# Optimization experiments

Measured on AMD Instinct MI355X. Metric: run time of the kernel, lower is better.

The kernel has to match this reference:

```python
import jax, jax.numpy as jnp
import numpy as np

N = 100000        # nodes
E = 1600000       # edges
DIM = 64
HEADS = 8
HEAD_DIM = DIM // HEADS
HIDDEN = 4 * DIM  # hidden_dim_multiplier = 4


def setup_inputs() -> dict:
    key = jax.random.key(0)
    ks = jax.random.split(key, 20)
    s = 0.05
    return {
        "x": jax.random.normal(ks[0], (N, DIM), jnp.float32),
        "edge_feat": jax.random.normal(ks[1], (E, 2), jnp.float32),
        "w_in": jax.random.normal(ks[2], (DIM, DIM), jnp.float32) * s,
        "b_in": jnp.zeros((DIM,), jnp.float32),
        "w_edge": jax.random.normal(ks[3], (2, DIM), jnp.float32) * s,
        "b_edge": jnp.zeros((DIM,), jnp.float32),
        "w_att_u": jax.random.normal(ks[4], (DIM, HEADS), jnp.float32) * s,
        "b_att_u": jnp.zeros((HEADS,), jnp.float32),
        "w_att_v": jax.random.normal(ks[5], (DIM, HEADS), jnp.float32) * s,  # no bias
        "w_att_e": jax.random.normal(ks[6], (DIM, HEADS), jnp.float32) * s,
        "b_att_e": jnp.zeros((HEADS,), jnp.float32),
        "w_ff1": jax.random.normal(ks[7], (DIM, HIDDEN), jnp.float32) * s,
        "b_ff1": jnp.zeros((HIDDEN,), jnp.float32),
        "w_ff2": jax.random.normal(ks[8], (HIDDEN, DIM), jnp.float32) * s,
        "b_ff2": jnp.zeros((DIM,), jnp.float32),
        "src": jax.random.randint(ks[9], (E,), 0, N, jnp.int32),
        "dst": jax.random.randint(ks[10], (E,), 0, N, jnp.int32),
    }


def reference(x, edge_feat, w_in, b_in, w_edge, b_edge, w_att_u, b_att_u,
              w_att_v, w_att_e, b_att_e, w_ff1, b_ff1, w_ff2, b_ff2, src, dst):
    n = x.shape[0]
    h = x @ w_in + b_in                                  # [N, dim]
    ea = edge_feat @ w_edge + b_edge                     # [E, dim]
    su = h @ w_att_u + b_att_u                           # [N, H]
    sv = h @ w_att_v                                     # [N, H] (no bias)
    se = ea @ w_att_e + b_att_e                          # [E, H]
    # u_add_v gather + edge bias + LeakyReLU
    scores = jax.nn.leaky_relu(su[src] + sv[dst] + se, 0.2)  # [E, H]
    # edge softmax over incoming edges of each dst node
    m = jax.ops.segment_max(scores, dst, num_segments=n)     # [N, H]
    m = jnp.where(jnp.isfinite(m), m, 0.0)                   # nodes w/o in-edges
    e = jnp.exp(scores - m[dst])                             # [E, H]
    denom = jax.ops.segment_sum(e, dst, num_segments=n)      # [N, H]
    probs = e / jnp.maximum(denom, 1e-12)[dst]               # [E, H]
    # u_mul_e_sum: weighted scatter-sum of messages
    hv = h.reshape(n, HEAD_DIM, HEADS)                       # [N, hd, H]
    msg = hv[src] * probs[:, None, :]                        # [E, hd, H]
    out = jax.ops.segment_sum(msg, dst, num_segments=n).reshape(n, DIM)
    # feed-forward (dropout=0 at eval)
    out = jax.nn.gelu(out @ w_ff1 + b_ff1, approximate=False) @ w_ff2 + b_ff2
    return out
```

## Files before the change

kernel.cpp:

```cpp
#include <hip/hip_runtime.h>
#include <math.h>

#define DIM 64
#define HEADS 8
#define HIDDEN 256

__device__ __forceinline__ float lane_bcast(float v, int srcLane) {
  return __int_as_float(__builtin_amdgcn_readlane(__float_as_int(v), srcLane));
}

__global__ void prep_kernel(
    const float* __restrict__ w_in, const float* __restrict__ b_in,
    const float* __restrict__ w_edge, const float* __restrict__ b_edge,
    const float* __restrict__ w_att_u, const float* __restrict__ b_att_u,
    const float* __restrict__ w_att_v,
    const float* __restrict__ w_att_e, const float* __restrict__ b_att_e,
    float* __restrict__ Waug, float* __restrict__ baug,
    float* __restrict__ wcc, float* __restrict__ bcc)
{
  int t = threadIdx.x;
  if (t < 64) {
    for (int j = 0; j < 64; ++j) Waug[t*80 + j] = w_in[t*64 + j];
    for (int hh = 0; hh < 8; ++hh) {
      float a = 0.f, b = 0.f;
      for (int j = 0; j < 64; ++j) {
        float w = w_in[t*64 + j];
        a += w * w_att_u[j*8 + hh];
        b += w * w_att_v[j*8 + hh];
      }
      Waug[t*80 + 64 + hh] = a;
      Waug[t*80 + 72 + hh] = b;
    }
  } else if (t < 128) {
    int j = t - 64;
    baug[j] = b_in[j];
  } else if (t < 136) {
    int hh = t - 128;
    float a = b_att_u[hh];
    for (int k = 0; k < 64; ++k) a += b_in[k] * w_att_u[k*8 + hh];
    baug[64 + hh] = a;
  } else if (t < 144) {
    int hh = t - 136;
    float a = 0.f;
    for (int k = 0; k < 64; ++k) a += b_in[k] * w_att_v[k*8 + hh];
    baug[72 + hh] = a;
  } else if (t < 160) {
    int c = (t - 144) >> 3, hh = (t - 144) & 7;
    float a = 0.f;
    for (int j = 0; j < 64; ++j) a += w_edge[c*64 + j] * w_att_e[j*8 + hh];
    wcc[c*8 + hh] = a;
  } else if (t < 168) {
    int hh = t - 160;
    float a = b_att_e[hh];
    for (int j = 0; j < 64; ++j) a += b_edge[j] * w_att_e[j*8 + hh];
    bcc[hh] = a;
  }
}

__global__ __launch_bounds__(256) void node_gemm_kernel(
    const float* __restrict__ x,
    const float* __restrict__ Waug, const float* __restrict__ baug,
    float* __restrict__ hbuf, float* __restrict__ subuf, float* __restrict__ svbuf,
    int n_nodes)
{
  const int wid = threadIdx.x >> 6;
  const int lane = threadIdx.x & 63;
  const long nbase = (long)blockIdx.x * 32 + wid * 8;

  float xr[8];
  #pragma unroll
  for (int m = 0; m < 8; ++m) {
    long n = nbase + m; if (n >= n_nodes) n = n_nodes - 1;
    xr[m] = x[n*DIM + lane];
  }
  const float bmain = baug[lane];
  const float bext  = (lane < 16) ? baug[64 + lane] : 0.f;
  float acc[8], acc2[8];
  #pragma unroll
  for (int m = 0; m < 8; ++m) { acc[m] = bmain; acc2[m] = 0.f; }

  #pragma unroll 16
  for (int k = 0; k < 64; ++k) {
    float wmain = Waug[k*80 + lane];
    float wext  = (lane < 16) ? Waug[k*80 + 64 + lane] : 0.f;
    #pragma unroll
    for (int m = 0; m < 8; ++m) {
      float xk = lane_bcast(xr[m], k);
      acc[m]  += xk * wmain;
      acc2[m] += xk * wext;
    }
  }
  #pragma unroll
  for (int m = 0; m < 8; ++m) {
    long n = nbase + m;
    if (n >= n_nodes) continue;
    hbuf[n*DIM + lane] = acc[m];
    if (lane < 8)       subuf[n*8 + lane]     = acc2[m] + bext;
    else if (lane < 16) svbuf[n*8 + lane - 8] = acc2[m] + bext;
  }
}

__global__ void hist_kernel(const int* __restrict__ dst, int* __restrict__ deg, int n_edges) {
  int i = blockIdx.x * blockDim.x + threadIdx.x;
  if (i < n_edges) atomicAdd(&deg[dst[i]], 1);
}

__global__ void alloc_kernel(const int* __restrict__ deg, int* __restrict__ off,
                             int* __restrict__ counter, int n_nodes) {
  int i = blockIdx.x * blockDim.x + threadIdx.x;
  int lane = threadIdx.x & 63;
  int d = (i < n_nodes) ? deg[i] : 0;
  int pre = d;
  #pragma unroll
  for (int s = 1; s < 64; s <<= 1) {
    int v = __shfl_up(pre, s, 64);
    if (lane >= s) pre += v;
  }
  int tot = __shfl(pre, 63, 64);
  int base = 0;
  if (lane == 0) base = atomicAdd(counter, tot);
  base = __shfl(base, 0, 64);
  if (i < n_nodes) off[i] = base + pre - d;
}

__global__ void scatter_kernel(const int* __restrict__ dst, const int* __restrict__ off,
                               int* __restrict__ pos, int* __restrict__ csr, int n_edges) {
  int i = blockIdx.x * blockDim.x + threadIdx.x;
  if (i < n_edges) {
    int d = dst[i];
    int p = atomicAdd(&pos[d], 1);
    csr[off[d] + p] = i;
  }
}

__device__ __forceinline__ float sel8(float v0, float v1, float v2, float v3,
                                      float v4, float v5, float v6, float v7, int idx) {
  float a0 = (idx & 1) ? v1 : v0;
  float a1 = (idx & 1) ? v3 : v2;
  float a2 = (idx & 1) ? v5 : v4;
  float a3 = (idx & 1) ? v7 : v6;
  float b0 = (idx & 2) ? a1 : a0;
  float b1 = (idx & 2) ? a3 : a2;
  return (idx & 4) ? b1 : b0;
}

__global__ __launch_bounds__(256) void attn_kernel(
    const int* __restrict__ src, const int* __restrict__ csr,
    const int* __restrict__ off, const int* __restrict__ deg,
    const float* __restrict__ edge_feat,
    const float* __restrict__ hbuf, const float* __restrict__ subuf,
    const float* __restrict__ svbuf,
    const float* __restrict__ wcc, const float* __restrict__ bcc,
    float* __restrict__ agg, int n_nodes)
{
  __shared__ float pbuf[4][64][8];
  __shared__ int   sbuf[4][64];
  const int wid = threadIdx.x >> 6;
  const int lane = threadIdx.x & 63;
  const long n = (long)blockIdx.x * 4 + wid;
  if (n >= n_nodes) return;
  const int ebase = off[n];
  const int d = deg[n];
  const int hsel = lane & 7;

  float svn[8], c0v[8], c1v[8], cbv[8];
  {
    const float4* svp = (const float4*)(svbuf + n*8);
    float4 s0 = svp[0], s1 = svp[1];
    svn[0]=s0.x; svn[1]=s0.y; svn[2]=s0.z; svn[3]=s0.w;
    svn[4]=s1.x; svn[5]=s1.y; svn[6]=s1.z; svn[7]=s1.w;
    #pragma unroll
    for (int hh = 0; hh < 8; ++hh) {
      c0v[hh] = wcc[hh]; c1v[hh] = wcc[8+hh]; cbv[hh] = bcc[hh];
    }
  }
  float m8[8], den8[8];
  #pragma unroll
  for (int hh = 0; hh < 8; ++hh) { m8[hh] = -INFINITY; den8[hh] = 0.f; }
  float msg = 0.f;

  for (int c0 = 0; c0 < d; c0 += 64) {
    const int cnt = min(64, d - c0);
    float sc[8];
    int sid = 0;
    if (lane < cnt) {
      const int eid = csr[ebase + c0 + lane];
      sid = src[eid];
      const float2 ef = *(const float2*)(edge_feat + (long)eid*2);
      const float4* sup = (const float4*)(subuf + (long)sid*8);
      float4 u0 = sup[0], u1 = sup[1];
      float suv[8] = {u0.x,u0.y,u0.z,u0.w,u1.x,u1.y,u1.z,u1.w};
      #pragma unroll
      for (int hh = 0; hh < 8; ++hh) {
        float v = suv[hh] + svn[hh] + ef.x*c0v[hh] + ef.y*c1v[hh] + cbv[hh];
        sc[hh] = (v > 0.f) ? v : 0.2f*v;
      }
    } else {
      #pragma unroll
      for (int hh = 0; hh < 8; ++hh) sc[hh] = -INFINITY;
    }
    float cm[8];
    #pragma unroll
    for (int hh = 0; hh < 8; ++hh) cm[hh] = sc[hh];
    #pragma unroll
    for (int sft = 32; sft >= 1; sft >>= 1) {
      #pragma unroll
      for (int hh = 0; hh < 8; ++hh)
        cm[hh] = fmaxf(cm[hh], __shfl_xor(cm[hh], sft, 64));
    }
    float f[8], pv[8];
    #pragma unroll
    for (int hh = 0; hh < 8; ++hh) {
      float nm = fmaxf(m8[hh], cm[hh]);
      f[hh] = __expf(m8[hh] - nm);
      pv[hh] = __expf(sc[hh] - nm);
      m8[hh] = nm;
    }
    if (lane < cnt) {
      float4* pp = (float4*)&pbuf[wid][lane][0];
      pp[0] = make_float4(pv[0], pv[1], pv[2], pv[3]);
      pp[1] = make_float4(pv[4], pv[5], pv[6], pv[7]);
      sbuf[wid][lane] = sid;
    }
    float q[8];
    #pragma unroll
    for (int hh = 0; hh < 8; ++hh) q[hh] = pv[hh];
    #pragma unroll
    for (int sft = 32; sft >= 1; sft >>= 1) {
      #pragma unroll
      for (int hh = 0; hh < 8; ++hh)
        q[hh] += __shfl_xor(q[hh], sft, 64);
    }
    #pragma unroll
    for (int hh = 0; hh < 8; ++hh) den8[hh] = den8[hh]*f[hh] + q[hh];
    msg *= sel8(f[0],f[1],f[2],f[3],f[4],f[5],f[6],f[7], hsel);

    asm volatile("s_waitcnt lgkmcnt(0)" ::: "memory");

    int e2 = 0;
    for (; e2 + 4 <= cnt; e2 += 4) {
      int s0 = sbuf[wid][e2],   s1 = sbuf[wid][e2+1];
      int s2 = sbuf[wid][e2+2], s3 = sbuf[wid][e2+3];
      float p0 = pbuf[wid][e2][hsel],   p1 = pbuf[wid][e2+1][hsel];
      float p2 = pbuf[wid][e2+2][hsel], p3 = pbuf[wid][e2+3][hsel];
      float h0 = hbuf[(long)s0*DIM + lane];
      float h1 = hbuf[(long)s1*DIM + lane];
      float h2 = hbuf[(long)s2*DIM + lane];
      float h3 = hbuf[(long)s3*DIM + lane];
      msg += h0*p0; msg += h1*p1; msg += h2*p2; msg += h3*p3;
    }
    for (; e2 < cnt; ++e2) {
      int s0 = sbuf[wid][e2];
      float p0 = pbuf[wid][e2][hsel];
      msg += hbuf[(long)s0*DIM + lane] * p0;
    }
  }
  float den = sel8(den8[0],den8[1],den8[2],den8[3],den8[4],den8[5],den8[6],den8[7], hsel);
  den = fmaxf(den, 1e-12f);
  agg[n*DIM + lane] = msg / den;
}

__global__ __launch_bounds__(256) void ffn_kernel(
    const float* __restrict__ agg,
    const float* __restrict__ w1, const float* __restrict__ b1,
    const float* __restrict__ w2, const float* __restrict__ b2,
    float* __restrict__ out, int n_nodes)
{
  __shared__ float hid[4][8][HIDDEN];
  const int wid = threadIdx.x >> 6;
  const int lane = threadIdx.x & 63;
  const long nbase = (long)blockIdx.x * 32 + wid * 8;

  float xr[8];
  #pragma unroll
  for (int m = 0; m < 8; ++m) {
    long n = nbase + m; if (n >= n_nodes) n = n_nodes - 1;
    xr[m] = agg[n*DIM + lane];
  }
  float4 bb = *(const float4*)(b1 + lane*4);
  float h[8][4];
  #pragma unroll
  for (int m = 0; m < 8; ++m) { h[m][0]=bb.x; h[m][1]=bb.y; h[m][2]=bb.z; h[m][3]=bb.w; }

  #pragma unroll 8
  for (int k = 0; k < 64; ++k) {
    float4 w = *(const float4*)(w1 + k*HIDDEN + lane*4);
    #pragma unroll
    for (int m = 0; m < 8; ++m) {
      float xk = lane_bcast(xr[m], k);
      h[m][0] += xk*w.x; h[m][1] += xk*w.y; h[m][2] += xk*w.z; h[m][3] += xk*w.w;
    }
  }
  #pragma unroll
  for (int m = 0; m < 8; ++m) {
    float4 g;
    g.x = 0.5f*h[m][0]*(1.0f + erff(h[m][0]*0.70710678118654752f));
    g.y = 0.5f*h[m][1]*(1.0f + erff(h[m][1]*0.70710678118654752f));
    g.z = 0.5f*h[m][2]*(1.0f + erff(h[m][2]*0.70710678118654752f));
    g.w = 0.5f*h[m][3]*(1.0f + erff(h[m][3]*0.70710678118654752f));
    *(float4*)&hid[wid][m][lane*4] = g;
  }
  asm volatile("s_waitcnt lgkmcnt(0)" ::: "memory");

  float acc[8];
  const float b2v = b2[lane];
  #pragma unroll
  for (int m = 0; m < 8; ++m) acc[m] = b2v;

  #pragma unroll 8
  for (int j4 = 0; j4 < 64; ++j4) {
    float wa = w2[(j4*4+0)*DIM + lane];
    float wb = w2[(j4*4+1)*DIM + lane];
    float wc = w2[(j4*4+2)*DIM + lane];
    float wd = w2[(j4*4+3)*DIM + lane];
    #pragma unroll
    for (int m = 0; m < 8; ++m) {
      float4 hv = *(const float4*)&hid[wid][m][j4*4];
      acc[m] += hv.x*wa + hv.y*wb + hv.z*wc + hv.w*wd;
    }
  }
  #pragma unroll
  for (int m = 0; m < 8; ++m) {
    long n = nbase + m;
    if (n < n_nodes) out[n*DIM + lane] = acc[m];
  }
}

extern "C" void kernel_launch(void* const* d_in, const int* in_sizes, int n_in,
                              void* d_out, int out_size, void* d_ws, size_t ws_size,
                              hipStream_t stream)
{
  const float* x         = (const float*)d_in[0];
  const float* edge_feat = (const float*)d_in[1];
  const float* w_in      = (const float*)d_in[2];
  const float* b_in      = (const float*)d_in[3];
  const float* w_edge    = (const float*)d_in[4];
  const float* b_edge    = (const float*)d_in[5];
  const float* w_att_u   = (const float*)d_in[6];
  const float* b_att_u   = (const float*)d_in[7];
  const float* w_att_v   = (const float*)d_in[8];
  const float* w_att_e   = (const float*)d_in[9];
  const float* b_att_e   = (const float*)d_in[10];
  const float* w_ff1     = (const float*)d_in[11];
  const float* b_ff1     = (const float*)d_in[12];
  const float* w_ff2     = (const float*)d_in[13];
  const float* b_ff2     = (const float*)d_in[14];
  const int*   src       = (const int*)d_in[15];
  const int*   dst       = (const int*)d_in[16];
  float* out = (float*)d_out;

  const int n_nodes = in_sizes[0] / DIM;
  const int n_edges = in_sizes[15];

  char* p = (char*)d_ws;
  auto alloc_f = [&](size_t cnt) { float* r = (float*)p; p += ((cnt*4 + 255) & ~(size_t)255); return r; };
  auto alloc_i = [&](size_t cnt) { int* r = (int*)p;   p += ((cnt*4 + 255) & ~(size_t)255); return r; };
  float* Waug  = alloc_f(64*80);
  float* baug  = alloc_f(80);
  float* wcc   = alloc_f(16);
  float* bcc   = alloc_f(8);
  float* hbuf  = alloc_f((size_t)n_nodes*DIM);
  float* subuf = alloc_f((size_t)n_nodes*8);
  float* svbuf = alloc_f((size_t)n_nodes*8);
  float* aggb  = alloc_f((size_t)n_nodes*DIM);
  int* deg     = alloc_i(n_nodes);
  int* pos     = alloc_i(n_nodes);
  int* counter = alloc_i(64);
  int* offb    = alloc_i(n_nodes);
  int* csr     = alloc_i(n_edges);

  hipMemsetAsync(deg, 0, (size_t)((char*)offb - (char*)deg), stream);

  hipLaunchKernelGGL(prep_kernel, dim3(1), dim3(256), 0, stream,
      w_in, b_in, w_edge, b_edge, w_att_u, b_att_u, w_att_v, w_att_e, b_att_e,
      Waug, baug, wcc, bcc);

  hipLaunchKernelGGL(node_gemm_kernel, dim3((n_nodes+31)/32), dim3(256), 0, stream,
      x, Waug, baug, hbuf, subuf, svbuf, n_nodes);

  hipLaunchKernelGGL(hist_kernel, dim3((n_edges+255)/256), dim3(256), 0, stream,
      dst, deg, n_edges);
  hipLaunchKernelGGL(alloc_kernel, dim3((n_nodes+255)/256), dim3(256), 0, stream,
      deg, offb, counter, n_nodes);
  hipLaunchKernelGGL(scatter_kernel, dim3((n_edges+255)/256), dim3(256), 0, stream,
      dst, offb, pos, csr, n_edges);

  hipLaunchKernelGGL(attn_kernel, dim3((n_nodes+3)/4), dim3(256), 0, stream,
      src, csr, offb, deg, edge_feat, hbuf, subuf, svbuf, wcc, bcc, aggb, n_nodes);

  hipLaunchKernelGGL(ffn_kernel, dim3((n_nodes+31)/32), dim3(256), 0, stream,
      aggb, w_ff1, b_ff1, w_ff2, b_ff2, out, n_nodes);
}
```

Measured before the change: 661.2 us.

## Pack four nodes per wavefront in attention and restructure FFN second GEMM

The attention kernel now assigns 16 lanes per destination node (four nodes per wavefront) instead of a full 64-lane wave. It processes edges in chunks of 16, and each lane gathers a float4 of h, which suits the average in-degree of 16 and cuts idle lanes and shuffle stages. The FFN kernel's second GEMM is rewritten so that each lane computes 8 outputs for one node, reading w2 as float4. The hidden activations are staged through a half-size padded LDS buffer in two halves. The restructuring raises per-lane register and global-load pressure, and the second GEMM now issues many more w2 loads per lane.

```diff
diff --git a/kernel.cpp b/kernel.cpp
--- a/kernel.cpp
+++ b/kernel.cpp
@@ -4,6 +4,7 @@
 #define DIM 64
 #define HEADS 8
 #define HIDDEN 256
+#define HPAD 132
 
 __device__ __forceinline__ float lane_bcast(float v, int srcLane) {
   return __int_as_float(__builtin_amdgcn_readlane(__float_as_int(v), srcLane));
@@ -133,17 +134,6 @@
   }
 }
 
-__device__ __forceinline__ float sel8(float v0, float v1, float v2, float v3,
-                                      float v4, float v5, float v6, float v7, int idx) {
-  float a0 = (idx & 1) ? v1 : v0;
-  float a1 = (idx & 1) ? v3 : v2;
-  float a2 = (idx & 1) ? v5 : v4;
-  float a3 = (idx & 1) ? v7 : v6;
-  float b0 = (idx & 2) ? a1 : a0;
-  float b1 = (idx & 2) ? a3 : a2;
-  return (idx & 4) ? b1 : b0;
-}
-
 __global__ __launch_bounds__(256) void attn_kernel(
     const int* __restrict__ src, const int* __restrict__ csr,
     const int* __restrict__ off, const int* __restrict__ deg,
@@ -153,19 +143,21 @@
     const float* __restrict__ wcc, const float* __restrict__ bcc,
     float* __restrict__ agg, int n_nodes)
 {
-  __shared__ float pbuf[4][64][8];
-  __shared__ int   sbuf[4][64];
+  __shared__ float pbuf[4][4][16][8];
+  __shared__ int   sbuf[4][4][16];
   const int wid = threadIdx.x >> 6;
   const int lane = threadIdx.x & 63;
-  const long n = (long)blockIdx.x * 4 + wid;
-  if (n >= n_nodes) return;
-  const int ebase = off[n];
-  const int d = deg[n];
-  const int hsel = lane & 7;
+  const int g = lane >> 4, sub = lane & 15;
+  const long n = (long)blockIdx.x * 16 + wid * 4 + g;
+  const bool valid = (n < n_nodes);
+  const long nc = valid ? n : (long)(n_nodes - 1);
+  const int ebase = off[nc];
+  const int d = valid ? deg[nc] : 0;
+  const int hb = (sub & 1) * 4;
 
   float svn[8], c0v[8], c1v[8], cbv[8];
   {
-    const float4* svp = (const float4*)(svbuf + n*8);
+    const float4* svp = (const float4*)(svbuf + nc*8);
     float4 s0 = svp[0], s1 = svp[1];
     svn[0]=s0.x; svn[1]=s0.y; svn[2]=s0.z; svn[3]=s0.w;
     svn[4]=s1.x; svn[5]=s1.y; svn[6]=s1.z; svn[7]=s1.w;
@@ -177,14 +169,14 @@
   float m8[8], den8[8];
   #pragma unroll
   for (int hh = 0; hh < 8; ++hh) { m8[hh] = -INFINITY; den8[hh] = 0.f; }
-  float msg = 0.f;
-
-  for (int c0 = 0; c0 < d; c0 += 64) {
-    const int cnt = min(64, d - c0);
+  float4 msg = make_float4(0.f, 0.f, 0.f, 0.f);
+
+  for (int c0 = 0; c0 < d; c0 += 16) {
+    const int cnt = min(16, d - c0);
     float sc[8];
     int sid = 0;
-    if (lane < cnt) {
-      const int eid = csr[ebase + c0 + lane];
+    if (sub < cnt) {
+      const int eid = csr[ebase + c0 + sub];
       sid = src[eid];
       const float2 ef = *(const float2*)(edge_feat + (long)eid*2);
       const float4* sup = (const float4*)(subuf + (long)sid*8);
@@ -203,7 +195,7 @@
     #pragma unroll
     for (int hh = 0; hh < 8; ++hh) cm[hh] = sc[hh];
     #pragma unroll
-    for (int sft = 32; sft >= 1; sft >>= 1) {
+    for (int sft = 8; sft >= 1; sft >>= 1) {
       #pragma unroll
       for (int hh = 0; hh < 8; ++hh)
         cm[hh] = fmaxf(cm[hh], __shfl_xor(cm[hh], sft, 64));
@@ -216,48 +208,52 @@
       pv[hh] = __expf(sc[hh] - nm);
       m8[hh] = nm;
     }
-    if (lane < cnt) {
-      float4* pp = (float4*)&pbuf[wid][lane][0];
+    if (sub < cnt) {
+      float4* pp = (float4*)&pbuf[wid][g][sub][0];
       pp[0] = make_float4(pv[0], pv[1], pv[2], pv[3]);
       pp[1] = make_float4(pv[4], pv[5], pv[6], pv[7]);
-      sbuf[wid][lane] = sid;
+      sbuf[wid][g][sub] = sid;
     }
     float q[8];
     #pragma unroll
     for (int hh = 0; hh < 8; ++hh) q[hh] = pv[hh];
     #pragma unroll
-    for (int sft = 32; sft >= 1; sft >>= 1) {
+    for (int sft = 8; sft >= 1; sft >>= 1) {
       #pragma unroll
       for (int hh = 0; hh < 8; ++hh)
         q[hh] += __shfl_xor(q[hh], sft, 64);
     }
     #pragma unroll
     for (int hh = 0; hh < 8; ++hh) den8[hh] = den8[hh]*f[hh] + q[hh];
-    msg *= sel8(f[0],f[1],f[2],f[3],f[4],f[5],f[6],f[7], hsel);
-
+    {
+      float f0 = (sub & 1) ? f[4] : f[0];
+      float f1 = (sub & 1) ? f[5] : f[1];
+      float f2 = (sub & 1) ? f[6] : f[2];
+      float f3 = (sub & 1) ? f[7] : f[3];
+      msg.x *= f0; msg.y *= f1; msg.z *= f2; msg.w *= f3;
+    }
     asm volatile("s_waitcnt lgkmcnt(0)" ::: "memory");
 
-    int e2 = 0;
-    for (; e2 + 4 <= cnt; e2 += 4) {
-      int s0 = sbuf[wid][e2],   s1 = sbuf[wid][e2+1];
-      int s2 = sbuf[wid][e2+2], s3 = sbuf[wid][e2+3];
-      float p0 = pbuf[wid][e2][hsel],   p1 = pbuf[wid][e2+1][hsel];
-      float p2 = pbuf[wid][e2+2][hsel], p3 = pbuf[wid][e2+3][hsel];
-      float h0 = hbuf[(long)s0*DIM + lane];
-      float h1 = hbuf[(long)s1*DIM + lane];
-      float h2 = hbuf[(long)s2*DIM + lane];
-      float h3 = hbuf[(long)s3*DIM + lane];
-      msg += h0*p0; msg += h1*p1; msg += h2*p2; msg += h3*p3;
-    }
-    for (; e2 < cnt; ++e2) {
-      int s0 = sbuf[wid][e2];
-      float p0 = pbuf[wid][e2][hsel];
-      msg += hbuf[(long)s0*DIM + lane] * p0;
-    }
-  }
-  float den = sel8(den8[0],den8[1],den8[2],den8[3],den8[4],den8[5],den8[6],den8[7], hsel);
-  den = fmaxf(den, 1e-12f);
-  agg[n*DIM + lane] = msg / den;
+    #pragma unroll 2
+    for (int e2 = 0; e2 < cnt; ++e2) {
+      int sidu = sbuf[wid][g][e2];
+      float4 p = *(const float4*)&pbuf[wid][g][e2][hb];
+      float4 hv = *(const float4*)&hbuf[(long)sidu*DIM + sub*4];
+      msg.x += hv.x*p.x; msg.y += hv.y*p.y; msg.z += hv.z*p.z; msg.w += hv.w*p.w;
+    }
+  }
+  float d0 = (sub & 1) ? den8[4] : den8[0];
+  float d1 = (sub & 1) ? den8[5] : den8[1];
+  float d2 = (sub & 1) ? den8[6] : den8[2];
+  float d3 = (sub & 1) ? den8[7] : den8[3];
+  if (valid) {
+    float4 o;
+    o.x = msg.x / fmaxf(d0, 1e-12f);
+    o.y = msg.y / fmaxf(d1, 1e-12f);
+    o.z = msg.z / fmaxf(d2, 1e-12f);
+    o.w = msg.w / fmaxf(d3, 1e-12f);
+    *(float4*)(agg + n*DIM + sub*4) = o;
+  }
 }
 
 __global__ __launch_bounds__(256) void ffn_kernel(
@@ -266,7 +262,7 @@
     const float* __restrict__ w2, const float* __restrict__ b2,
     float* __restrict__ out, int n_nodes)
 {
-  __shared__ float hid[4][8][HIDDEN];
+  __shared__ float hid[4][8][HPAD];
   const int wid = threadIdx.x >> 6;
   const int lane = threadIdx.x & 63;
   const long nbase = (long)blockIdx.x * 32 + wid * 8;
@@ -293,36 +289,66 @@
   }
   #pragma unroll
   for (int m = 0; m < 8; ++m) {
-    float4 g;
-    g.x = 0.5f*h[m][0]*(1.0f + erff(h[m][0]*0.70710678118654752f));
-    g.y = 0.5f*h[m][1]*(1.0f + erff(h[m][1]*0.70710678118654752f));
-    g.z = 0.5f*h[m][2]*(1.0f + erff(h[m][2]*0.70710678118654752f));
-    g.w = 0.5f*h[m][3]*(1.0f + erff(h[m][3]*0.70710678118654752f));
-    *(float4*)&hid[wid][m][lane*4] = g;
-  }
+    #pragma unroll
+    for (int i = 0; i < 4; ++i)
+      h[m][i] = 0.5f*h[m][i]*(1.0f + erff(h[m][i]*0.70710678118654752f));
+  }
+
+  if (lane < 32) {
+    #pragma unroll
+    for (int m = 0; m < 8; ++m)
+      *(float4*)&hid[wid][m][lane*4] = make_float4(h[m][0], h[m][1], h[m][2], h[m][3]);
+  }
+  asm volatile("" ::: "memory");
   asm volatile("s_waitcnt lgkmcnt(0)" ::: "memory");
 
-  float acc[8];
-  const float b2v = b2[lane];
-  #pragma unroll
-  for (int m = 0; m < 8; ++m) acc[m] = b2v;
-
-  #pragma unroll 8
-  for (int j4 = 0; j4 < 64; ++j4) {
-    float wa = w2[(j4*4+0)*DIM + lane];
-    float wb = w2[(j4*4+1)*DIM + lane];
-    float wc = w2[(j4*4+2)*DIM + lane];
-    float wd = w2[(j4*4+3)*DIM + lane];
-    #pragma unroll
-    for (int m = 0; m < 8; ++m) {
-      float4 hv = *(const float4*)&hid[wid][m][j4*4];
-      acc[m] += hv.x*wa + hv.y*wb + hv.z*wc + hv.w*wd;
-    }
-  }
-  #pragma unroll
-  for (int m = 0; m < 8; ++m) {
-    long n = nbase + m;
-    if (n < n_nodes) out[n*DIM + lane] = acc[m];
+  const int mi = lane >> 3, dg = lane & 7;
+  float4 accA = *(const float4*)(b2 + dg*8);
+  float4 accB = *(const float4*)(b2 + dg*8 + 4);
+
+  #pragma unroll 4
+  for (int jc = 0; jc < 32; ++jc) {
+    float4 hv = *(const float4*)&hid[wid][mi][jc*4];
+    float hvv[4] = {hv.x, hv.y, hv.z, hv.w};
+    #pragma unroll
+    for (int jj = 0; jj < 4; ++jj) {
+      int j = jc*4 + jj;
+      float4 wA = *(const float4*)(w2 + j*DIM + dg*8);
+      float4 wB = *(const float4*)(w2 + j*DIM + dg*8 + 4);
+      float hvj = hvv[jj];
+      accA.x += hvj*wA.x; accA.y += hvj*wA.y; accA.z += hvj*wA.z; accA.w += hvj*wA.w;
+      accB.x += hvj*wB.x; accB.y += hvj*wB.y; accB.z += hvj*wB.z; accB.w += hvj*wB.w;
+    }
+  }
+
+  asm volatile("" ::: "memory");
+  if (lane >= 32) {
+    #pragma unroll
+    for (int m = 0; m < 8; ++m)
+      *(float4*)&hid[wid][m][(lane-32)*4] = make_float4(h[m][0], h[m][1], h[m][2], h[m][3]);
+  }
+  asm volatile("" ::: "memory");
+  asm volatile("s_waitcnt lgkmcnt(0)" ::: "memory");
+
+  #pragma unroll 4
+  for (int jc = 0; jc < 32; ++jc) {
+    float4 hv = *(const float4*)&hid[wid][mi][jc*4];
+    float hvv[4] = {hv.x, hv.y, hv.z, hv.w};
+    #pragma unroll
+    for (int jj = 0; jj < 4; ++jj) {
+      int j = 128 + jc*4 + jj;
+      float4 wA = *(const float4*)(w2 + j*DIM + dg*8);
+      float4 wB = *(const float4*)(w2 + j*DIM + dg*8 + 4);
+      float hvj = hvv[jj];
+      accA.x += hvj*wA.x; accA.y += hvj*wA.y; accA.z += hvj*wA.z; accA.w += hvj*wA.w;
+      accB.x += hvj*wB.x; accB.y += hvj*wB.y; accB.z += hvj*wB.z; accB.w += hvj*wB.w;
+    }
+  }
+
+  long n = nbase + mi;
+  if (n < n_nodes) {
+    *(float4*)(out + n*DIM + dg*8)     = accA;
+    *(float4*)(out + n*DIM + dg*8 + 4) = accB;
   }
 }
 
@@ -385,7 +411,7 @@
   hipLaunchKernelGGL(scatter_kernel, dim3((n_edges+255)/256), dim3(256), 0, stream,
       dst, offb, pos, csr, n_edges);
 
-  hipLaunchKernelGGL(attn_kernel, dim3((n_nodes+3)/4), dim3(256), 0, stream,
+  hipLaunchKernelGGL(attn_kernel, dim3((n_nodes+15)/16), dim3(256), 0, stream,
       src, csr, offb, deg, edge_feat, hbuf, subuf, svbuf, wcc, bcc, aggb, n_nodes);
 
   hipLaunchKernelGGL(ffn_kernel, dim3((n_nodes+31)/32), dim3(256), 0, stream,
```

Measured after the change: 719.1 us. +8.8%, slower.
